# Kernel tuning notes

Hardware: AMD Instinct MI355X
Metric: run time of the kernel (lower is better)

## Reference

```python
import jax, jax.numpy as jnp
import numpy as np

N = 50000      # nodes
E = 800000     # edges
IN = 128       # in_dim
OUT = 64       # out_dim
NEG_SLOPE = 0.01  # F.leaky_relu default


def setup_inputs() -> dict:
    key = jax.random.key(0)
    k1, k2, k3, k4, k5 = jax.random.split(key, 5)
    h = jax.random.normal(k1, (N, IN), dtype=jnp.float32)
    # xavier-normal-ish scale for the two linear layers
    W_fc = jax.random.normal(k2, (OUT, IN), dtype=jnp.float32) * (2.0 / (IN + OUT)) ** 0.5
    W_attn = jax.random.normal(k3, (2 * OUT,), dtype=jnp.float32) * (2.0 / (2 * OUT + 1)) ** 0.5
    src = jax.random.randint(k4, (E,), 0, N)
    dst = jax.random.randint(k5, (E,), 0, N)
    return {"h": h, "W_fc": W_fc, "W_attn": W_attn, "src": src, "dst": dst}


def reference(h, W_fc, W_attn, src, dst):
    # z = fc(h): [N, OUT]
    z = jnp.einsum("ni,oi->no", h, W_fc)
    d = z.shape[-1]
    # per-edge attention logit: attn_fc(cat([z_src, z_dst])) == z_src@a_l + z_dst@a_r
    a_l, a_r = W_attn[:d], W_attn[d:]
    zs = z[src]                                   # [E, OUT] gather
    e = jax.nn.leaky_relu(zs @ a_l + z[dst] @ a_r, negative_slope=NEG_SLOPE)  # [E]
    # segment softmax over incoming edges of each dst node
    m = jax.ops.segment_max(e, dst, num_segments=N)          # [N]
    ex = jnp.exp(e - m[dst])                                  # [E]
    denom = jax.ops.segment_sum(ex, dst, num_segments=N)      # [N]
    alpha = ex / denom[dst]                                    # [E]
    # weighted scatter-sum of source features
    out = jax.ops.segment_sum(alpha[:, None] * zs, dst, num_segments=N)  # [N, OUT]
    return out
```

## Files before the change

### kernel.cpp

```cpp
#include <hip/hip_runtime.h>
#include <hip/hip_bf16.h>
#include <math.h>

#define IN_DIM 128
#define OUT_DIM 64
#define NEG_SLOPE 0.01f
#define BCAP 1536
#define P1_EPT 16
#define P1_THREADS 1024
#define P1_EDGES (P1_THREADS * P1_EPT)

typedef __attribute__((ext_vector_type(8))) short bf8_t;
typedef __attribute__((ext_vector_type(4))) float f4_t;

__device__ __forceinline__ bf8_t pack8(float4 a, float4 b) {
    union { bf8_t v; __hip_bfloat162 h[4]; } u;
    u.h[0] = __float22bfloat162_rn(make_float2(a.x, a.y));
    u.h[1] = __float22bfloat162_rn(make_float2(a.z, a.w));
    u.h[2] = __float22bfloat162_rn(make_float2(b.x, b.y));
    u.h[3] = __float22bfloat162_rn(make_float2(b.z, b.w));
    return u.v;
}

__global__ __launch_bounds__(1024) void k_front(
    const int* __restrict__ src, const int* __restrict__ dst,
    int* __restrict__ bucket_cursor, unsigned* __restrict__ tmp, int E,
    const float4* __restrict__ h4, const float4* __restrict__ W4,
    const float* __restrict__ Wattn,
    __hip_bfloat16* __restrict__ zb, float* __restrict__ s_l, float* __restrict__ s_r,
    int N, int NP1)
{
    __shared__ int cntA[1024];
    __shared__ int sbase[1024];
    __shared__ int gbaseS[1024];
    __shared__ int wsum[17];
    __shared__ unsigned sortedE[P1_EDGES];

    const int t = threadIdx.x;

    if (blockIdx.x < NP1) {
        const int base_e = blockIdx.x * P1_EDGES;

        cntA[t] = 0;
        __syncthreads();

        unsigned pArr[P1_EPT];
        unsigned short rArr[P1_EPT];
        #pragma unroll
        for (int i = 0; i < P1_EPT; i++) {
            int ei = base_e + i * P1_THREADS + t;
            if (ei < E) {
                int s = src[ei], d = dst[ei];
                int b = d >> 6;
                pArr[i] = ((unsigned)b << 22) | ((unsigned)s << 6) | (unsigned)(d & 63);
                rArr[i] = (unsigned short)atomicAdd(&cntA[b], 1);
            } else {
                pArr[i] = 0xFFFFFFFFu;
            }
        }
        __syncthreads();

        const int c = cntA[t];
        int gb = (c > 0) ? atomicAdd(&bucket_cursor[t], c) : 0;

        const int lane = t & 63, wv = t >> 6;
        int inc = c;
        #pragma unroll
        for (int o = 1; o < 64; o <<= 1) {
            int v = __shfl_up(inc, o, 64);
            if (lane >= o) inc += v;
        }
        if (lane == 63) wsum[wv] = inc;
        __syncthreads();
        if (t < 16) {
            int wval = wsum[t];
            int winc = wval;
            #pragma unroll
            for (int o = 1; o < 16; o <<= 1) {
                int v = __shfl_up(winc, o, 64);
                if (t >= o) winc += v;
            }
            wsum[t] = winc - wval;
        }
        __syncthreads();
        sbase[t] = wsum[wv] + (inc - c);
        __syncthreads();

        #pragma unroll
        for (int i = 0; i < P1_EPT; i++) {
            unsigned p = pArr[i];
            if (p == 0xFFFFFFFFu) continue;
            int b = p >> 22;
            sortedE[sbase[b] + rArr[i]] = p;
        }
        gbaseS[t] = gb;
        __syncthreads();

        const int total = sbase[1023] + cntA[1023];
        for (int i = t; i < total; i += P1_THREADS) {
            unsigned p = sortedE[i];
            int b = p >> 22;
            int slot = gbaseS[b] + (i - sbase[b]);
            if (slot < BCAP)
                tmp[(size_t)b * BCAP + slot] = p;
        }
    } else {
        const int lane = t & 63;
        const int wv   = t >> 6;
        const int col  = lane & 15, quad = lane >> 4;
        const int n0   = (blockIdx.x - NP1) * 256 + wv * 16;
        if (n0 >= N) return;

        bf8_t bf[4][4];
        #pragma unroll
        for (int ns = 0; ns < 4; ns++) {
            const float4* wrow = W4 + (size_t)(ns * 16 + col) * (IN_DIM / 4);
            #pragma unroll
            for (int kb = 0; kb < 4; kb++) {
                float4 x = wrow[kb * 8 + quad * 2];
                float4 y = wrow[kb * 8 + quad * 2 + 1];
                bf[kb][ns] = pack8(x, y);
            }
        }

        const int  na = n0 + col;
        const bool nv = (na < N);
        const float4* hrow = h4 + (size_t)(nv ? na : 0) * (IN_DIM / 4);
        const float4 zero = make_float4(0.f, 0.f, 0.f, 0.f);

        f4_t acc[4];
        #pragma unroll
        for (int ns = 0; ns < 4; ns++) acc[ns] = (f4_t){0.f, 0.f, 0.f, 0.f};

        #pragma unroll
        for (int kb = 0; kb < 4; kb++) {
            float4 x = nv ? hrow[kb * 8 + quad * 2]     : zero;
            float4 y = nv ? hrow[kb * 8 + quad * 2 + 1] : zero;
            bf8_t a = pack8(x, y);
            #pragma unroll
            for (int ns = 0; ns < 4; ns++)
                acc[ns] = __builtin_amdgcn_mfma_f32_16x16x32_bf16(a, bf[kb][ns], acc[ns], 0, 0, 0);
        }

        float alv[4], arv[4];
        #pragma unroll
        for (int ns = 0; ns < 4; ns++) {
            alv[ns] = Wattn[ns * 16 + col];
            arv[ns] = Wattn[OUT_DIM + ns * 16 + col];
        }
        #pragma unroll
        for (int r = 0; r < 4; r++) {
            const int nn = n0 + quad * 4 + r;
            float pl = acc[0][r] * alv[0] + acc[1][r] * alv[1] + acc[2][r] * alv[2] + acc[3][r] * alv[3];
            float pr = acc[0][r] * arv[0] + acc[1][r] * arv[1] + acc[2][r] * arv[2] + acc[3][r] * arv[3];
            #pragma unroll
            for (int o = 1; o < 16; o <<= 1) {
                pl += __shfl_xor(pl, o, 64);
                pr += __shfl_xor(pr, o, 64);
            }
            if (nn < N) {
                __hip_bfloat16* zr = zb + (size_t)nn * OUT_DIM;
                #pragma unroll
                for (int ns = 0; ns < 4; ns++)
                    zr[ns * 16 + col] = __float2bfloat16(acc[ns][r]);
                if (col == 0) { s_l[nn] = pl; s_r[nn] = pr; }
            }
        }
    }
}

__global__ __launch_bounds__(256) void k_tail(
    const unsigned* __restrict__ tmp, const int* __restrict__ bucket_cnt,
    const float* __restrict__ s_l, const float* __restrict__ s_r,
    const uint4* __restrict__ zb4, float4* __restrict__ out4, int N)
{
    __shared__ uint2 se[BCAP];
    __shared__ unsigned p2s[BCAP];
    __shared__ float exs[BCAP];
    __shared__ int cnt_s[64], off_s[64];
    __shared__ float srs[64];

    const int b = blockIdx.x, t = threadIdx.x;
    const int lane = t & 63;
    const int nbase = b * 64;
    int mb = bucket_cnt[b];
    if (mb > BCAP) mb = BCAP;

    if (t < 64) {
        cnt_s[t] = 0;
        int n = nbase + t;
        srs[t] = (n < N) ? s_r[n] : 0.f;
    }
    __syncthreads();

    const unsigned* mybuf = tmp + (size_t)b * BCAP;

    const int mb4 = mb & ~3;
    for (int i0 = t * 4; i0 < mb4; i0 += 256 * 4) {
        uint4 pv = *reinterpret_cast<const uint4*>(mybuf + i0);
        #pragma unroll
        for (int j = 0; j < 4; j++) {
            unsigned p = (j == 0) ? pv.x : (j == 1) ? pv.y : (j == 2) ? pv.z : pv.w;
            int i = i0 + j;
            int d = p & 63u;
            int s = (p >> 6) & 0xFFFFu;
            float e = s_l[s] + srs[d];
            e = (e > 0.f) ? e : NEG_SLOPE * e;
            float ex = __expf(e);
            int r = atomicAdd(&cnt_s[d], 1);
            if (r > 1023) r = 1023;
            p2s[i] = ((unsigned)r << 22) | (p & 0x3FFFFFu);
            exs[i] = ex;
        }
    }
    for (int i = mb4 + t; i < mb; i += 256) {
        unsigned p = mybuf[i];
        int d = p & 63u;
        int s = (p >> 6) & 0xFFFFu;
        float e = s_l[s] + srs[d];
        e = (e > 0.f) ? e : NEG_SLOPE * e;
        float ex = __expf(e);
        int r = atomicAdd(&cnt_s[d], 1);
        if (r > 1023) r = 1023;
        p2s[i] = ((unsigned)r << 22) | (p & 0x3FFFFFu);
        exs[i] = ex;
    }
    __syncthreads();

    if (t < 64) {
        int c = cnt_s[t];
        int inc = c;
        #pragma unroll
        for (int o = 1; o < 64; o <<= 1) {
            int v = __shfl_up(inc, o, 64);
            if (lane >= o) inc += v;
        }
        off_s[t] = inc - c;
    }
    __syncthreads();

    for (int i = t; i < mb; i += 256) {
        unsigned q = p2s[i];
        int d = q & 63u;
        int slot = off_s[d] + (int)(q >> 22);
        if (slot < BCAP)
            se[slot] = make_uint2((q >> 6) & 0xFFFFu, __float_as_uint(exs[i]));
    }
    __syncthreads();

    const int ch8 = t & 7;
    const int grp = t >> 3;

    for (int nl = grp; nl < 64; nl += 32) {
        const int n = nbase + nl;
        if (n >= N) continue;
        const int beg = off_s[nl];
        int end = beg + cnt_s[nl];
        if (end > BCAP) end = BCAP;
        float4* op = out4 + (size_t)n * 16 + ch8 * 2;

        if (end <= beg) {
            op[0] = make_float4(0.f, 0.f, 0.f, 0.f);
            op[1] = make_float4(0.f, 0.f, 0.f, 0.f);
            continue;
        }

        float a0 = 0.f, a1 = 0.f, a2 = 0.f, a3 = 0.f;
        float a4 = 0.f, a5 = 0.f, a6 = 0.f, a7 = 0.f;
        float dsum = 0.f;

        #pragma unroll 8
        for (int i = beg; i < end; ++i) {
            uint2 q = se[i];
            float ex = __uint_as_float(q.y);
            dsum += ex;
            uint4 zv = zb4[(size_t)q.x * 8 + ch8];
            float f0 = __uint_as_float(zv.x << 16);
            float f1 = __uint_as_float(zv.x & 0xffff0000u);
            float f2 = __uint_as_float(zv.y << 16);
            float f3 = __uint_as_float(zv.y & 0xffff0000u);
            float f4 = __uint_as_float(zv.z << 16);
            float f5 = __uint_as_float(zv.z & 0xffff0000u);
            float f6 = __uint_as_float(zv.w << 16);
            float f7 = __uint_as_float(zv.w & 0xffff0000u);
            a0 += ex * f0; a1 += ex * f1; a2 += ex * f2; a3 += ex * f3;
            a4 += ex * f4; a5 += ex * f5; a6 += ex * f6; a7 += ex * f7;
        }

        float inv = 1.f / dsum;
        op[0] = make_float4(a0 * inv, a1 * inv, a2 * inv, a3 * inv);
        op[1] = make_float4(a4 * inv, a5 * inv, a6 * inv, a7 * inv);
    }
}

extern "C" void kernel_launch(void* const* d_in, const int* in_sizes, int n_in,
                              void* d_out, int out_size, void* d_ws, size_t ws_size,
                              hipStream_t stream)
{
    const float* h     = (const float*)d_in[0];
    const float* Wfc   = (const float*)d_in[1];
    const float* Wattn = (const float*)d_in[2];
    const int*   src   = (const int*)d_in[3];
    const int*   dst   = (const int*)d_in[4];
    const int N = in_sizes[0] / IN_DIM;
    const int E = in_sizes[3];
    const int NBK = (N + 63) / 64;
    const int NP1 = (E + P1_EDGES - 1) / P1_EDGES;

    __hip_bfloat16* zb = (__hip_bfloat16*)d_ws;
    float* s_l     = (float*)(zb + (size_t)N * OUT_DIM);
    float* s_r     = s_l + N;
    int*   bcursor = (int*)(s_r + N);
    unsigned* tmp  = (unsigned*)(bcursor + 1024);

    const int nblk_g = (N + 255) / 256;

    hipMemsetAsync(bcursor, 0, 1024 * sizeof(int), stream);

    k_front<<<NP1 + nblk_g, P1_THREADS, 0, stream>>>(src, dst, bcursor, tmp, E,
                                              (const float4*)h, (const float4*)Wfc, Wattn,
                                              zb, s_l, s_r, N, NP1);
    k_tail <<<NBK, 256, 0, stream>>>(tmp, bcursor, s_l, s_r,
                                     (const uint4*)zb, (float4*)d_out, N);
}
```

Before: 138.7 us.

## Shrink front kernel blocks to 256 threads, each handling four dst buckets

Reduces k_front block size from 1024 to 256 threads. In the bucketing path each thread now owns four buckets, with a vectorized count load, four cursor atomics and a simpler two-level prefix scan. The GEMM path covers 64 nodes per block, so more blocks are launched. Smaller blocks with a smaller per-block shared sortedE array should let more blocks fit per CU and improve scheduling. The trade-off is more blocks and more global cursor atomics, and each bucket gets a smaller edge chunk per block.

```diff
diff --git a/kernel.cpp b/kernel.cpp
--- a/kernel.cpp
+++ b/kernel.cpp
@@ -7,7 +7,7 @@
 #define NEG_SLOPE 0.01f
 #define BCAP 1536
 #define P1_EPT 16
-#define P1_THREADS 1024
+#define P1_THREADS 256
 #define P1_EDGES (P1_THREADS * P1_EPT)
 
 typedef __attribute__((ext_vector_type(8))) short bf8_t;
@@ -22,7 +22,7 @@
     return u.v;
 }
 
-__global__ __launch_bounds__(1024) void k_front(
+__global__ __launch_bounds__(256) void k_front(
     const int* __restrict__ src, const int* __restrict__ dst,
     int* __restrict__ bucket_cursor, unsigned* __restrict__ tmp, int E,
     const float4* __restrict__ h4, const float4* __restrict__ W4,
@@ -33,7 +33,7 @@
     __shared__ int cntA[1024];
     __shared__ int sbase[1024];
     __shared__ int gbaseS[1024];
-    __shared__ int wsum[17];
+    __shared__ int wsum[4];
     __shared__ unsigned sortedE[P1_EDGES];
 
     const int t = threadIdx.x;
@@ -41,14 +41,14 @@
     if (blockIdx.x < NP1) {
         const int base_e = blockIdx.x * P1_EDGES;
 
-        cntA[t] = 0;
+        for (int b = t; b < 1024; b += 256) cntA[b] = 0;
         __syncthreads();
 
         unsigned pArr[P1_EPT];
         unsigned short rArr[P1_EPT];
         #pragma unroll
         for (int i = 0; i < P1_EPT; i++) {
-            int ei = base_e + i * P1_THREADS + t;
+            int ei = base_e + i * 256 + t;
             if (ei < E) {
                 int s = src[ei], d = dst[ei];
                 int b = d >> 6;
@@ -60,11 +60,17 @@
         }
         __syncthreads();
 
-        const int c = cntA[t];
-        int gb = (c > 0) ? atomicAdd(&bucket_cursor[t], c) : 0;
+        const int4 cv = *reinterpret_cast<const int4*>(&cntA[t * 4]);
+        const int c0 = cv.x, c1 = cv.y, c2 = cv.z, c3 = cv.w;
+        const int csum = c0 + c1 + c2 + c3;
+
+        int g0 = (c0 > 0) ? atomicAdd(&bucket_cursor[t * 4 + 0], c0) : 0;
+        int g1 = (c1 > 0) ? atomicAdd(&bucket_cursor[t * 4 + 1], c1) : 0;
+        int g2 = (c2 > 0) ? atomicAdd(&bucket_cursor[t * 4 + 2], c2) : 0;
+        int g3 = (c3 > 0) ? atomicAdd(&bucket_cursor[t * 4 + 3], c3) : 0;
 
         const int lane = t & 63, wv = t >> 6;
-        int inc = c;
+        int inc = csum;
         #pragma unroll
         for (int o = 1; o < 64; o <<= 1) {
             int v = __shfl_up(inc, o, 64);
@@ -72,18 +78,14 @@
         }
         if (lane == 63) wsum[wv] = inc;
         __syncthreads();
-        if (t < 16) {
-            int wval = wsum[t];
-            int winc = wval;
-            #pragma unroll
-            for (int o = 1; o < 16; o <<= 1) {
-                int v = __shfl_up(winc, o, 64);
-                if (t >= o) winc += v;
-            }
-            wsum[t] = winc - wval;
-        }
-        __syncthreads();
-        sbase[t] = wsum[wv] + (inc - c);
+        int wb = 0;
+        #pragma unroll
+        for (int j = 0; j < 4; j++) if (j < wv) wb += wsum[j];
+        const int base = wb + inc - csum;
+        sbase[t * 4 + 0] = base;
+        sbase[t * 4 + 1] = base + c0;
+        sbase[t * 4 + 2] = base + c0 + c1;
+        sbase[t * 4 + 3] = base + c0 + c1 + c2;
         __syncthreads();
 
         #pragma unroll
@@ -93,11 +95,14 @@
             int b = p >> 22;
             sortedE[sbase[b] + rArr[i]] = p;
         }
-        gbaseS[t] = gb;
+        gbaseS[t * 4 + 0] = g0;
+        gbaseS[t * 4 + 1] = g1;
+        gbaseS[t * 4 + 2] = g2;
+        gbaseS[t * 4 + 3] = g3;
         __syncthreads();
 
         const int total = sbase[1023] + cntA[1023];
-        for (int i = t; i < total; i += P1_THREADS) {
+        for (int i = t; i < total; i += 256) {
             unsigned p = sortedE[i];
             int b = p >> 22;
             int slot = gbaseS[b] + (i - sbase[b]);
@@ -108,7 +113,7 @@
         const int lane = t & 63;
         const int wv   = t >> 6;
         const int col  = lane & 15, quad = lane >> 4;
-        const int n0   = (blockIdx.x - NP1) * 256 + wv * 16;
+        const int n0   = (blockIdx.x - NP1) * 64 + wv * 16;
         if (n0 >= N) return;
 
         bf8_t bf[4][4];
@@ -313,7 +318,7 @@
     int*   bcursor = (int*)(s_r + N);
     unsigned* tmp  = (unsigned*)(bcursor + 1024);
 
-    const int nblk_g = (N + 255) / 256;
+    const int nblk_g = (N + 63) / 64;
 
     hipMemsetAsync(bcursor, 0, 1024 * sizeof(int), stream);
 
```

Result: slower. 143.3 us (+3.3%).
